# Optimization experiments

Measured on AMD Instinct MI355X. Metric: run time of the kernel, lower is better.

The kernel has to match this reference:

```python
import jax, jax.numpy as jnp
import numpy as np


def conv1x1(x, w, bias):
    # x: [B,C,H,W], w: [O,C], bias: [O]
    return jnp.einsum('bchw,oc->bohw', x, w) + bias[None, :, None, None]


def setup_inputs() -> dict:
    key = jax.random.key(0)
    ks = jax.random.split(key, 12)
    B, Cin_half, H, W = 8, 128, 128, 128
    Cin, Cout = 256, 256
    s_in = 1.0 / np.sqrt(Cin)
    s_out = 1.0 / np.sqrt(Cout)
    return {
        'a': jax.random.normal(ks[0], (B, Cin_half, H, W), jnp.float32),
        'b': jax.random.normal(ks[1], (B, Cin_half, H, W), jnp.float32),
        'w1': jax.random.uniform(ks[2], (Cout, Cin), jnp.float32, -s_in, s_in),
        'b1': jax.random.uniform(ks[3], (Cout,), jnp.float32, -s_in, s_in),
        'w2': jax.random.uniform(ks[4], (Cout, Cout), jnp.float32, -s_out, s_out),
        'b2': jax.random.uniform(ks[5], (Cout,), jnp.float32, -s_out, s_out),
        'w3': jax.random.uniform(ks[6], (Cout, Cout), jnp.float32, -s_out, s_out),
        'b3': jax.random.uniform(ks[7], (Cout,), jnp.float32, -s_out, s_out),
        'w4': jax.random.uniform(ks[8], (Cout, Cout), jnp.float32, -s_out, s_out),
        'b4': jax.random.uniform(ks[9], (Cout,), jnp.float32, -s_out, s_out),
    }


def reference(a, b, w1, b1, w2, b2, w3, b3, w4, b4):
    z = jnp.concatenate([a, b], axis=1)            # [B, Cin, H, W]
    z = conv1x1(z, w1, b1)                          # [B, C, H, W]
    B, C, H, W = z.shape
    q = conv1x1(z, w2, b2).reshape(B, C, H * W)     # [B, C, N]
    k = conv1x1(z, w3, b3).reshape(B, C, H * W)
    v = conv1x1(z, w4, b4).reshape(B, C, H * W)
    qk = jnp.einsum('bcn,bdn->bcd', q, k)           # [B, C, C] (q @ k^T)
    attn = jax.nn.softmax(qk, axis=-1)
    out = jnp.einsum('bcd,bdn->bcn', attn, v)       # [B, C, N]
    return out.reshape(B, C, H, W)
```

## Files before the change

kernel.cpp:

```cpp
#include <hip/hip_runtime.h>

typedef float  f4v  __attribute__((ext_vector_type(4)));
typedef __bf16 bf8v __attribute__((ext_vector_type(8)));
typedef unsigned int u32x2 __attribute__((ext_vector_type(2)));
typedef unsigned int u32x4 __attribute__((ext_vector_type(4)));
typedef unsigned short u16;

#define MFMA(a,b,c) __builtin_amdgcn_mfma_f32_16x16x32_bf16((a),(b),(c),0,0,0)
#define HW_N 16384

__device__ __forceinline__ u16 bf_rne(float x){
  unsigned u = __float_as_uint(x);
  u += 0x7fffu + ((u >> 16) & 1u);
  return (u16)(u >> 16);
}

__global__ void k_weights(const float* __restrict__ w1, const float* __restrict__ b1,
                          const float* __restrict__ w2, const float* __restrict__ b2,
                          const float* __restrict__ w3, const float* __restrict__ b3,
                          const float* __restrict__ w4, const float* __restrict__ b4,
                          float* __restrict__ Wq, float* __restrict__ WkT,
                          float* __restrict__ Wv, float* __restrict__ bq,
                          float* __restrict__ bk, float* __restrict__ bv)
{
  const int blk = blockIdx.x, t = threadIdx.x;
  if (blk == 96){
    float aq = 0.f, ak = 0.f, av = 0.f;
    for (int j = 0; j < 256; ++j){
      const float bb = b1[j];
      aq += w2[t*256 + j] * bb;
      ak += w3[t*256 + j] * bb;
      av += w4[t*256 + j] * bb;
    }
    bq[t] = aq + b2[t];
    bk[t] = ak + b3[t];
    bv[t] = av + b4[t];
    return;
  }
  for (int i = 0; i < 8; ++i){
    const int e   = blk*2048 + i*256 + t;
    const int mat = e >> 16;
    const int c   = (e >> 8) & 255;
    const int col = e & 255;
    const float* wsrc = (mat == 0) ? w2 : ((mat == 1) ? w3 : w4);
    float acc = 0.f;
    for (int j = 0; j < 256; ++j) acc += wsrc[c*256 + j] * w1[j*256 + col];
    if      (mat == 0) Wq [c*256 + col] = acc;
    else if (mat == 1) WkT[col*256 + c] = acc;
    else               Wv [c*256 + col] = acc;
  }
}

__global__ __launch_bounds__(512, 2) void k_gram(
    const float* __restrict__ xa, const float* __restrict__ xb,
    float* __restrict__ Gpart, float* __restrict__ spart)
{
  __shared__ u16 hbuf[2][256*64];
  __shared__ u16 lbuf[2][256*64];
  const int blk = blockIdx.x;
  const int b = blk >> 5, half = (blk >> 4) & 1, chunk = blk & 15;
  const int t = threadIdx.x;
  const int lane = t & 63, w = t >> 6;
  const int wr = w >> 1, wc = w & 1;
  const int c4 = t & 15, crow = t >> 4;

  const float* rowp[8];
#pragma unroll
  for (int p = 0; p < 8; ++p){
    const int c = crow + 32*p;
    const float* base = (c < 128) ? (xa + (size_t)(b*128 + c) * HW_N)
                                  : (xb + (size_t)(b*128 + (c-128)) * HW_N);
    rowp[p] = base + c4*4;
  }

  float ssum[8];
#pragma unroll
  for (int p = 0; p < 8; ++p) ssum[p] = 0.f;

  const f4v vzero = {0.f, 0.f, 0.f, 0.f};
  f4v acc[4][4];
#pragma unroll
  for (int i = 0; i < 4; ++i)
#pragma unroll
    for (int j = 0; j < 4; ++j) acc[i][j] = vzero;

  f4v ld[8];
  auto issue = [&](int s){
    const int n0 = chunk*1024 + s*64;
#pragma unroll
    for (int p = 0; p < 8; ++p) ld[p] = *(const f4v*)(rowp[p] + n0);
  };
  auto wbuf = [&](int bi){
#pragma unroll
    for (int p = 0; p < 8; ++p){
      const int c = crow + 32*p;
      const f4v v = ld[p];
      ssum[p] += (v[0] + v[1]) + (v[2] + v[3]);
      u16 h[4], l[4];
#pragma unroll
      for (int i = 0; i < 4; ++i){
        const float x = v[i];
        const u16 hb = bf_rne(x);
        const float hf = __uint_as_float(((unsigned)hb) << 16);
        h[i] = hb; l[i] = bf_rne(x - hf);
      }
      u32x2 hp, lp;
      hp[0] = (unsigned)h[0] | ((unsigned)h[1] << 16);
      hp[1] = (unsigned)h[2] | ((unsigned)h[3] << 16);
      lp[0] = (unsigned)l[0] | ((unsigned)l[1] << 16);
      lp[1] = (unsigned)l[2] | ((unsigned)l[3] << 16);
      const int off = c*64 + (((c4 >> 1) ^ (c & 7)) * 8) + (c4 & 1) * 4;
      *(u32x2*)&hbuf[bi][off] = hp;
      *(u32x2*)&lbuf[bi][off] = lp;
    }
  };
  auto mstep = [&](int bi){
#pragma unroll
    for (int kk = 0; kk < 2; ++kk){
      bf8v ah[4], al[4], bh[4], bl[4];
#pragma unroll
      for (int f = 0; f < 4; ++f){
        const int so = kk*4 + (lane >> 4);
        const int r  = wr*64 + f*16 + (lane & 15);
        const int oa = r*64 + ((so ^ (r & 7)) * 8);
        ah[f] = *(const bf8v*)&hbuf[bi][oa];
        al[f] = *(const bf8v*)&lbuf[bi][oa];
        const int rc = 128*half + wc*64 + f*16 + (lane & 15);
        const int ob = rc*64 + ((so ^ (rc & 7)) * 8);
        bh[f] = *(const bf8v*)&hbuf[bi][ob];
        bl[f] = *(const bf8v*)&lbuf[bi][ob];
      }
#pragma unroll
      for (int i = 0; i < 4; ++i)
#pragma unroll
        for (int j = 0; j < 4; ++j){
          acc[i][j] = MFMA(ah[i], bh[j], acc[i][j]);
          acc[i][j] = MFMA(ah[i], bl[j], acc[i][j]);
          acc[i][j] = MFMA(al[i], bh[j], acc[i][j]);
        }
    }
  };

  issue(0); wbuf(0); __syncthreads();
  for (int s = 0; s < 16; ++s){
    const int cur = s & 1;
    if (s < 15) issue(s + 1);
    mstep(cur);
    if (s < 15) wbuf(cur ^ 1);
    __syncthreads();
  }

  float* gp = Gpart + (size_t)((b*2 + half)*16 + chunk) * 32768;
#pragma unroll
  for (int i = 0; i < 4; ++i)
#pragma unroll
    for (int j = 0; j < 4; ++j){
      const int row = wr*64 + i*16 + ((lane >> 4) << 2);
      const int col = wc*64 + j*16 + (lane & 15);
#pragma unroll
      for (int r2 = 0; r2 < 4; ++r2)
        gp[(row + r2)*128 + col] = acc[i][j][r2];
    }

  if (half == 0){
#pragma unroll
    for (int p = 0; p < 8; ++p){
      float v = ssum[p];
      v += __shfl_xor(v, 1);
      v += __shfl_xor(v, 2);
      v += __shfl_xor(v, 4);
      v += __shfl_xor(v, 8);
      if ((lane & 15) == 0)
        spart[(b*16 + chunk)*256 + (crow + 32*p)] = v;
    }
  }
}

__global__ void k_redg(const float* __restrict__ Gpart, float* __restrict__ G)
{
  for (int k = 0; k < 8; ++k){
    const int o = blockIdx.x*2048 + k*256 + threadIdx.x;
    const int b = o >> 16, r = (o >> 8) & 255, col = o & 255;
    const int half = col >> 7, cc = col & 127;
    const float* p = Gpart + (size_t)(b*2 + half)*524288 + (size_t)r*128 + cc;
    float s = 0.f;
#pragma unroll
    for (int ch = 0; ch < 16; ++ch) s += p[ch*32768];
    G[o] = s;
  }
}

__device__ __forceinline__ float block_red(float v, int ismax, volatile float* red, int t){
#pragma unroll
  for (int m = 32; m; m >>= 1){
    const float o = __shfl_xor(v, m);
    v = ismax ? fmaxf(v, o) : (v + o);
  }
  if ((t & 63) == 0) red[t >> 6] = v;
  __syncthreads();
  const float r01 = ismax ? fmaxf(red[0], red[1]) : (red[0] + red[1]);
  const float r23 = ismax ? fmaxf(red[2], red[3]) : (red[2] + red[3]);
  v = ismax ? fmaxf(r01, r23) : (r01 + r23);
  __syncthreads();
  return v;
}

__global__ __launch_bounds__(256, 2) void k_attn(
    const float* __restrict__ G, const float* __restrict__ spart,
    const float* __restrict__ Wq, const float* __restrict__ WkT,
    const float* __restrict__ Wv, const float* __restrict__ bq,
    const float* __restrict__ bk, const float* __restrict__ bv,
    u16* __restrict__ Mfrag, float* __restrict__ cb)
{
  __shared__ float s_lds[256];
  __shared__ float wq_lds[4][256];
  __shared__ float t1_lds[4][256];
  __shared__ float a_lds[4][256];
  __shared__ float red[4];
  const int blk = blockIdx.x;
  const int b = blk >> 6, r0 = (blk & 63) * 4;
  const int t = threadIdx.x;

  float sv = 0.f;
#pragma unroll
  for (int ch = 0; ch < 16; ++ch) sv += spart[(b*16 + ch)*256 + t];
  s_lds[t] = sv;
#pragma unroll
  for (int ri = 0; ri < 4; ++ri) wq_lds[ri][t] = Wq[(r0 + ri)*256 + t];
  __syncthreads();

  float t1[4] = {0,0,0,0}, pv[4] = {0,0,0,0};
  const float* gb = G + (size_t)b * 65536;
  for (int k = 0; k < 256; ++k){
    const float g  = gb[k*256 + t];
    const float sk = s_lds[k];
#pragma unroll
    for (int ri = 0; ri < 4; ++ri){
      const float wqv = wq_lds[ri][k];
      t1[ri] += wqv * g;
      pv[ri] += wqv * sk;
    }
  }
#pragma unroll
  for (int ri = 0; ri < 4; ++ri) t1_lds[ri][t] = t1[ri];
  __syncthreads();

  float qk[4] = {0,0,0,0}, rd = 0.f;
  for (int n = 0; n < 256; ++n){
    const float wkt = WkT[n*256 + t];
    rd += wkt * s_lds[n];
#pragma unroll
    for (int ri = 0; ri < 4; ++ri) qk[ri] += t1_lds[ri][n] * wkt;
  }
  const float bkv = bk[t];
#pragma unroll
  for (int ri = 0; ri < 4; ++ri){
    const float bqv = bq[r0 + ri];
    qk[ri] += pv[ri]*bkv + bqv*rd + 16384.f*bqv*bkv;
  }

  float areg[4];
#pragma unroll
  for (int ri = 0; ri < 4; ++ri){
    const float m = block_red(qk[ri], 1, red, t);
    const float e = __expf(qk[ri] - m);
    const float s = block_red(e, 0, red, t);
    areg[ri] = e / s;
    a_lds[ri][t] = areg[ri];
  }
  const float bvv = bv[t];
#pragma unroll
  for (int ri = 0; ri < 4; ++ri){
    const float c = block_red(areg[ri]*bvv, 0, red, t);
    if (t == 0) cb[b*256 + r0 + ri] = c;
  }
  __syncthreads();

  float m4[4] = {0,0,0,0};
  for (int d = 0; d < 256; ++d){
    const float wv = Wv[d*256 + t];
#pragma unroll
    for (int ri = 0; ri < 4; ++ri) m4[ri] += a_lds[ri][d] * wv;
  }
  const int ks = t >> 5, lhi = (t >> 3) & 3, j = t & 7;
#pragma unroll
  for (int ri = 0; ri < 4; ++ri){
    const int o = r0 + ri;
    Mfrag[(size_t)b*65536 +
          (size_t)((((o >> 4)*8 + ks)*64) + (o & 15) + (lhi << 4))*8 + j] = bf_rne(m4[ri]);
  }
}

__global__ __launch_bounds__(512, 4) void k_out(
    const float* __restrict__ xa, const float* __restrict__ xb,
    const u16* __restrict__ Mfrag, const float* __restrict__ cb,
    float* __restrict__ out)
{
  __shared__ u16 xt[2][32*256];
  const int blk = blockIdx.x;
  const int b = blk >> 6, nchunk = blk & 63;
  const int t = threadIdx.x;
  const int lane = t & 63, w = t >> 6;
  const int cr = t >> 1;
  const int hf = t & 1;

  u32x4 af[2][8];
  const u16* mb = Mfrag + (size_t)b * 65536;
#pragma unroll
  for (int f = 0; f < 2; ++f)
#pragma unroll
    for (int ks = 0; ks < 8; ++ks)
      af[f][ks] = *(const u32x4*)(mb + (size_t)((((w*2 + f)*8 + ks)*64 + lane))*8);
#pragma unroll
  for (int f = 0; f < 2; ++f)
#pragma unroll
    for (int ks = 0; ks < 8; ++ks)
      asm volatile("" : "+a"(af[f][ks]));

  f4v cb4[2];
#pragma unroll
  for (int f = 0; f < 2; ++f)
    cb4[f] = *(const f4v*)(cb + b*256 + w*32 + f*16 + ((lane >> 4) << 2));

  const float* rowbase = (cr < 128) ? (xa + (size_t)(b*128 + cr)*HW_N)
                                    : (xb + (size_t)(b*128 + (cr-128))*HW_N);
  const float* rp = rowbase + hf*16;

  f4v ld[4];
  auto issue = [&](int s){
    const int n0 = nchunk*256 + s*32;
#pragma unroll
    for (int q = 0; q < 4; ++q) ld[q] = *(const f4v*)(rp + n0 + q*4);
  };
  auto cvtwrite = [&](int bi){
#pragma unroll
    for (int q = 0; q < 4; ++q){
      const f4v v = ld[q];
#pragma unroll
      for (int i = 0; i < 4; ++i){
        const int n = hf*16 + q*4 + i;
        xt[bi][n*256 + (((cr >> 3) ^ (n & 15))*8) + (cr & 7)] = bf_rne(v[i]);
      }
    }
  };

  const f4v vzero = {0.f, 0.f, 0.f, 0.f};
  float* outp = out + (size_t)b*256*HW_N;

  issue(0);
  cvtwrite(0);
  __syncthreads();

  for (int s = 0; s < 8; ++s){
    const int cur = s & 1;
    if (s < 7) issue(s + 1);

    const int n0 = nchunk*256 + s*32;
    f4v acc[2][2];
#pragma unroll
    for (int f = 0; f < 2; ++f){ acc[f][0] = vzero; acc[f][1] = vzero; }

#pragma unroll
    for (int ks = 0; ks < 8; ++ks){
      bf8v bfr[2];
#pragma unroll
      for (int g = 0; g < 2; ++g){
        const int n  = g*16 + (lane & 15);
        const int so = ks*4 + (lane >> 4);
        bfr[g] = *(const bf8v*)&xt[cur][n*256 + ((so ^ (n & 15))*8)];
      }
#pragma unroll
      for (int f = 0; f < 2; ++f){
        acc[f][0] = MFMA(__builtin_bit_cast(bf8v, af[f][ks]), bfr[0], acc[f][0]);
        acc[f][1] = MFMA(__builtin_bit_cast(bf8v, af[f][ks]), bfr[1], acc[f][1]);
      }
    }

#pragma unroll
    for (int f = 0; f < 2; ++f)
#pragma unroll
      for (int g = 0; g < 2; ++g){
        const int row = w*32 + f*16 + ((lane >> 4) << 2);
        const int col = n0 + g*16 + (lane & 15);
#pragma unroll
        for (int r2 = 0; r2 < 4; ++r2)
          outp[(size_t)(row + r2)*HW_N + col] = acc[f][g][r2] + cb4[f][r2];
      }

    if (s < 7) cvtwrite(cur ^ 1);
    __syncthreads();
  }
}

extern "C" void kernel_launch(void* const* d_in, const int* in_sizes, int n_in,
                              void* d_out, int out_size, void* d_ws, size_t ws_size,
                              hipStream_t stream)
{
  const float* xa = (const float*)d_in[0];
  const float* xb = (const float*)d_in[1];
  const float* w1 = (const float*)d_in[2];
  const float* b1 = (const float*)d_in[3];
  const float* w2 = (const float*)d_in[4];
  const float* b2 = (const float*)d_in[5];
  const float* w3 = (const float*)d_in[6];
  const float* b3 = (const float*)d_in[7];
  const float* w4 = (const float*)d_in[8];
  const float* b4 = (const float*)d_in[9];
  float* out = (float*)d_out;
  char*  ws  = (char*)d_ws;

  float* Gpart = (float*)(ws + 0);
  float* G     = (float*)(ws + 33554432);
  float* spart = (float*)(ws + 35651584);
  float* Wq    = (float*)(ws + 35782656);
  float* WkT   = (float*)(ws + 36044800);
  float* Wv    = (float*)(ws + 36306944);
  float* bq    = (float*)(ws + 36569088);
  float* bk    = (float*)(ws + 36570112);
  float* bv    = (float*)(ws + 36571136);
  u16*   Mfrag = (u16*)  (ws + 36572160);
  float* cb    = (float*)(ws + 37620736);

  hipLaunchKernelGGL(k_weights, dim3(97),  dim3(256), 0, stream,
                     w1,b1,w2,b2,w3,b3,w4,b4, Wq,WkT,Wv,bq,bk,bv);
  hipLaunchKernelGGL(k_gram,    dim3(256), dim3(512), 0, stream, xa, xb, Gpart, spart);
  hipLaunchKernelGGL(k_redg,    dim3(256), dim3(256), 0, stream, Gpart, G);
  hipLaunchKernelGGL(k_attn,    dim3(512), dim3(256), 0, stream,
                     G, spart, Wq, WkT, Wv, bq, bk, bv, Mfrag, cb);
  hipLaunchKernelGGL(k_out,     dim3(512), dim3(512), 0, stream, xa, xb, Mfrag, cb, out);
}
```

Before: 248.5 us.

## Stash bf16 input copy in gram kernel and read it in output GEMM

The gram kernel now writes the bf16 high part of the concatenated input to a workspace buffer while it is already converting tiles. A new output kernel reads this half-size bf16 tensor instead of the fp32 inputs, and the old fp32 kernel stays as a fallback when the workspace is too small. This trades extra write traffic in the gram pass for halved read traffic in the output pass, relying on cache residency to come out ahead.

```diff
diff --git a/kernel.cpp b/kernel.cpp
--- a/kernel.cpp
+++ b/kernel.cpp
@@ -5,6 +5,7 @@
 typedef unsigned int u32x2 __attribute__((ext_vector_type(2)));
 typedef unsigned int u32x4 __attribute__((ext_vector_type(4)));
 typedef unsigned short u16;
+typedef unsigned short u16x8 __attribute__((ext_vector_type(8)));
 
 #define MFMA(a,b,c) __builtin_amdgcn_mfma_f32_16x16x32_bf16((a),(b),(c),0,0,0)
 #define HW_N 16384
@@ -53,7 +54,8 @@
 
 __global__ __launch_bounds__(512, 2) void k_gram(
     const float* __restrict__ xa, const float* __restrict__ xb,
-    float* __restrict__ Gpart, float* __restrict__ spart)
+    float* __restrict__ Gpart, float* __restrict__ spart,
+    u16* __restrict__ xbf)
 {
   __shared__ u16 hbuf[2][256*64];
   __shared__ u16 lbuf[2][256*64];
@@ -90,7 +92,7 @@
 #pragma unroll
     for (int p = 0; p < 8; ++p) ld[p] = *(const f4v*)(rowp[p] + n0);
   };
-  auto wbuf = [&](int bi){
+  auto wbuf = [&](int bi, int s){
 #pragma unroll
     for (int p = 0; p < 8; ++p){
       const int c = crow + 32*p;
@@ -112,6 +114,9 @@
       const int off = c*64 + (((c4 >> 1) ^ (c & 7)) * 8) + (c4 & 1) * 4;
       *(u32x2*)&hbuf[bi][off] = hp;
       *(u32x2*)&lbuf[bi][off] = lp;
+      if (xbf && half == 0){
+        *(u32x2*)&xbf[(size_t)(b*256 + c)*HW_N + chunk*1024 + s*64 + c4*4] = hp;
+      }
     }
   };
   auto mstep = [&](int bi){
@@ -141,12 +146,12 @@
     }
   };
 
-  issue(0); wbuf(0); __syncthreads();
+  issue(0); wbuf(0, 0); __syncthreads();
   for (int s = 0; s < 16; ++s){
     const int cur = s & 1;
     if (s < 15) issue(s + 1);
     mstep(cur);
-    if (s < 15) wbuf(cur ^ 1);
+    if (s < 15) wbuf(cur ^ 1, s + 1);
     __syncthreads();
   }
 
@@ -292,6 +297,106 @@
 }
 
 __global__ __launch_bounds__(512, 4) void k_out(
+    const u16* __restrict__ xbf, const u16* __restrict__ Mfrag,
+    const float* __restrict__ cb, float* __restrict__ out)
+{
+  __shared__ u16 xt[2][64*256];
+  const int blk = blockIdx.x;
+  const int b = blk >> 6, nchunk = blk & 63;
+  const int t = threadIdx.x;
+  const int lane = t & 63, w = t >> 6;
+
+  u32x4 af[2][8];
+  const u16* mb = Mfrag + (size_t)b * 65536;
+#pragma unroll
+  for (int f = 0; f < 2; ++f)
+#pragma unroll
+    for (int ks = 0; ks < 8; ++ks)
+      af[f][ks] = *(const u32x4*)(mb + (size_t)(((w*2 + f)*8 + ks)*64 + lane)*8);
+#pragma unroll
+  for (int f = 0; f < 2; ++f)
+#pragma unroll
+    for (int ks = 0; ks < 8; ++ks)
+      asm volatile("" : "+a"(af[f][ks]));
+
+  float cbv[2];
+#pragma unroll
+  for (int f = 0; f < 2; ++f)
+    cbv[f] = cb[b*256 + w*32 + f*16 + (lane & 15)];
+
+  const int oct = t & 7, cr0 = t >> 3;
+  const u16* xp = xbf + (size_t)b*256*HW_N + (size_t)cr0*HW_N + nchunk*256 + oct*8;
+
+  u16x8 ld[4];
+  auto issue = [&](int s){
+#pragma unroll
+    for (int q = 0; q < 4; ++q)
+      ld[q] = *(const u16x8*)(xp + (size_t)q*64*HW_N + s*64);
+  };
+  auto swrite = [&](int bi){
+#pragma unroll
+    for (int q = 0; q < 4; ++q){
+      const int c = cr0 + 64*q;
+#pragma unroll
+      for (int j = 0; j < 8; ++j){
+        const int n = oct*8 + j;
+        xt[bi][n*256 + (((c >> 3) ^ (n & 15))*8) + (c & 7)] = ld[q][j];
+      }
+    }
+  };
+
+  const f4v vzero = {0.f, 0.f, 0.f, 0.f};
+  float* outp = out + (size_t)b*256*HW_N;
+
+  issue(0);
+  swrite(0);
+  __syncthreads();
+
+  for (int s = 0; s < 4; ++s){
+    const int cur = s & 1;
+    if (s < 3) issue(s + 1);
+
+    const int n0 = nchunk*256 + s*64;
+#pragma unroll
+    for (int gh = 0; gh < 2; ++gh){
+      f4v acc[2][2];
+#pragma unroll
+      for (int f = 0; f < 2; ++f){ acc[f][0] = vzero; acc[f][1] = vzero; }
+
+#pragma unroll
+      for (int ks = 0; ks < 8; ++ks){
+        bf8v xf[2];
+#pragma unroll
+        for (int g2 = 0; g2 < 2; ++g2){
+          const int n  = (gh*2 + g2)*16 + (lane & 15);
+          const int so = ks*4 + (lane >> 4);
+          xf[g2] = *(const bf8v*)&xt[cur][n*256 + ((so ^ (n & 15))*8)];
+        }
+#pragma unroll
+        for (int f = 0; f < 2; ++f){
+          acc[f][0] = MFMA(xf[0], __builtin_bit_cast(bf8v, af[f][ks]), acc[f][0]);
+          acc[f][1] = MFMA(xf[1], __builtin_bit_cast(bf8v, af[f][ks]), acc[f][1]);
+        }
+      }
+
+#pragma unroll
+      for (int f = 0; f < 2; ++f){
+        const int row = w*32 + f*16 + (lane & 15);
+#pragma unroll
+        for (int g2 = 0; g2 < 2; ++g2){
+          const int px = n0 + (gh*2 + g2)*16 + ((lane >> 4) << 2);
+          f4v v = acc[f][g2] + cbv[f];
+          *(f4v*)&outp[(size_t)row*HW_N + px] = v;
+        }
+      }
+    }
+
+    if (s < 3) swrite(cur ^ 1);
+    __syncthreads();
+  }
+}
+
+__global__ __launch_bounds__(512, 4) void k_out_f32(
     const float* __restrict__ xa, const float* __restrict__ xb,
     const u16* __restrict__ Mfrag, const float* __restrict__ cb,
     float* __restrict__ out)
@@ -420,12 +525,19 @@
   float* bv    = (float*)(ws + 36571136);
   u16*   Mfrag = (u16*)  (ws + 36572160);
   float* cb    = (float*)(ws + 37620736);
+  const size_t XBF_OFF  = 37628928;
+  const size_t WS_NEED  = XBF_OFF + 67108864;
+  const bool   use_bf   = ws_size >= WS_NEED;
+  u16*   xbf   = use_bf ? (u16*)(ws + XBF_OFF) : (u16*)nullptr;
 
   hipLaunchKernelGGL(k_weights, dim3(97),  dim3(256), 0, stream,
                      w1,b1,w2,b2,w3,b3,w4,b4, Wq,WkT,Wv,bq,bk,bv);
-  hipLaunchKernelGGL(k_gram,    dim3(256), dim3(512), 0, stream, xa, xb, Gpart, spart);
+  hipLaunchKernelGGL(k_gram,    dim3(256), dim3(512), 0, stream, xa, xb, Gpart, spart, xbf);
   hipLaunchKernelGGL(k_redg,    dim3(256), dim3(256), 0, stream, Gpart, G);
   hipLaunchKernelGGL(k_attn,    dim3(512), dim3(256), 0, stream,
                      G, spart, Wq, WkT, Wv, bq, bk, bv, Mfrag, cb);
-  hipLaunchKernelGGL(k_out,     dim3(512), dim3(512), 0, stream, xa, xb, Mfrag, cb, out);
-}
+  if (use_bf)
+    hipLaunchKernelGGL(k_out,     dim3(512), dim3(512), 0, stream, xbf, Mfrag, cb, out);
+  else
+    hipLaunchKernelGGL(k_out_f32, dim3(512), dim3(512), 0, stream, xa, xb, Mfrag, cb, out);
+}
```

Result: slower. 294.5 us (+18.5%).
